# Optimization experiments

Measured on AMD Instinct MI355X. Metric: run time of the kernel, lower is better.

Reference implementation:

```python
import jax, jax.numpy as jnp
import numpy as np

C = 51  # num_relation


def setup_inputs() -> dict:
    key = jax.random.key(0)
    N_o, N_u, D = 16384, 16384, 1024
    k = jax.random.split(key, 6)
    feat = jax.random.normal(k[0], (N_o + N_u, D), jnp.float32)
    # first N_o rows are labeled (label != 0), remaining N_u rows unlabeled (label == 0)
    label = jnp.concatenate([
        jax.random.randint(k[1], (N_o,), 1, C),
        jnp.zeros((N_u,), jnp.int32),
    ]).astype(jnp.int32)
    W_o = jax.random.normal(k[2], (C, D), jnp.float32) * 0.03
    b_o = jnp.zeros((C,), jnp.float32)
    W = jax.random.normal(k[3], (C, D), jnp.float32) * 0.03
    b = jnp.zeros((C,), jnp.float32)
    cls = jnp.arange(C)
    group_mid_mask = (cls >= 16) & (cls < 36)   # groups[1]
    group_tail_mask = cls >= 36                 # groups[2]
    # runtime torch.randint partner sampling, hoisted to input construction
    idx_m = jax.random.randint(k[4], (2, N_u), 0, N_o)  # 2 mid copies
    idx_t = jax.random.randint(k[5], (3, N_u), 0, N_o)  # 3 tail copies
    return dict(feat=feat, label=label, W_o=W_o, b_o=b_o, W=W, b=b,
                group_mid_mask=group_mid_mask, group_tail_mask=group_tail_mask,
                idx_m=idx_m, idx_t=idx_t)


def reference(feat, label, W_o, b_o, W, b, group_mid_mask, group_tail_mask, idx_m, idx_t):
    n_u = idx_m.shape[1]
    n_o = feat.shape[0] - n_u
    feat_o, feat_u = feat[:n_o], feat[n_o:]
    label_o = label[:n_o]

    # fc_o under no_grad, then softmax / top-1 rank + score
    logits = jax.lax.stop_gradient(feat_u @ W_o.T + b_o)      # [N_u, C]
    p = jax.nn.softmax(logits, axis=1)
    pred = jnp.argmax(p, axis=1)                               # ranks[:,0]
    score = jnp.max(p, axis=1)                                 # score[:,0]

    # group membership + confidence thresholds (heads are unused in the original)
    mid_m = group_mid_mask[pred] & (score > 0.5)
    tail_m = group_tail_mask[pred] & (score > 0.3)

    oh_u = jax.nn.one_hot(pred, C, dtype=feat.dtype)
    oh_o = jax.nn.one_hot(label_o, C, dtype=feat.dtype)

    im = idx_m.reshape(-1)   # [2*N_u]
    it = idx_t.reshape(-1)   # [3*N_u]

    fm = 0.7 * feat_o[im] + 0.3 * jnp.tile(feat_u, (2, 1))
    lm = 0.7 * oh_o[im] + 0.3 * jnp.tile(oh_u, (2, 1))
    ft = 0.7 * feat_o[it] + 0.3 * jnp.tile(feat_u, (3, 1))
    lt = 0.7 * oh_o[it] + 0.3 * jnp.tile(oh_u, (3, 1))

    feat_cat = jnp.concatenate([fm, ft], axis=0)               # [5*N_u, D]
    label_cat = jnp.concatenate([lm, lt], axis=0)              # [5*N_u, C]
    w = jnp.concatenate([jnp.tile(mid_m, 2), jnp.tile(tail_m, 3)]).astype(feat.dtype)

    # soft-label cross entropy on fc(feat_cat); masked mean over selected rows
    logp = jax.nn.log_softmax(feat_cat @ W.T + b, axis=1)
    ce = -(logp * label_cat).sum(axis=1)
    cnt = w.sum()
    return (ce * w).sum() / jnp.maximum(cnt, 1.0)
```

## Files before the change

### kernel.cpp

```cpp
#include <hip/hip_runtime.h>
#include <math.h>

#define DD 1024
#define NU 16384
#define NO 16384

typedef short short8 __attribute__((ext_vector_type(8)));
typedef float f32x4 __attribute__((ext_vector_type(4)));

__device__ __forceinline__ unsigned short f2b(float x) {
    unsigned int u = __float_as_uint(x);
    u += 0x7FFFu + ((u >> 16) & 1u);
    return (unsigned short)(u >> 16);
}

__device__ __forceinline__ short8 cvt8(float4 a, float4 b) {
    short8 r;
    r[0] = (short)f2b(a.x); r[1] = (short)f2b(a.y);
    r[2] = (short)f2b(a.z); r[3] = (short)f2b(a.w);
    r[4] = (short)f2b(b.x); r[5] = (short)f2b(b.y);
    r[6] = (short)f2b(b.z); r[7] = (short)f2b(b.w);
    return r;
}

__global__ __launch_bounds__(256) void fused(const float* __restrict__ feat,
                                             const float* __restrict__ W_o,
                                             const float* __restrict__ b_o,
                                             const float* __restrict__ W,
                                             const float* __restrict__ bb,
                                             const int* __restrict__ label,
                                             const int* __restrict__ idxm,
                                             const int* __restrict__ idxt,
                                             double* __restrict__ pnum,
                                             int* __restrict__ pcnt) {
    __shared__ __attribute__((aligned(16))) unsigned short Bs[32][64][32];
    __shared__ int2 slist[192];
    __shared__ int scount;
    __shared__ float swsum[4];
    __shared__ int swcnt[4];

    const int tid = threadIdx.x;
    const int lane = tid & 63;
    const int w = tid >> 6;
    const int m = lane & 15;
    const int quad = lane >> 4;

    if (tid == 0) scount = 0;

#pragma unroll 8
    for (int i = tid; i < 51 * 256; i += 256) {
        const int row = i >> 8;
        const int c = i & 255;
        const int k0 = c * 4;
        const int kt = k0 >> 5;
        const int kl = k0 & 31;
        const int c4 = kl >> 3;
        const int half = (kl >> 2) & 1;
        const float4 v = *(const float4*)(W_o + (size_t)row * DD + k0);
        ushort4 o;
        o.x = f2b(v.x); o.y = f2b(v.y); o.z = f2b(v.z); o.w = f2b(v.w);
        char* dst = (char*)&Bs[kt][row][0] + ((c4 ^ (row & 3)) * 16 + half * 8);
        *(ushort4*)dst = o;
    }
#pragma unroll 4
    for (int i = tid; i < 13 * 256; i += 256) {
        const int row = 51 + (i >> 8);
        const int j = i & 255;
        char* dst = (char*)&Bs[j >> 3][row][0] + (j & 7) * 8;
        *(ushort4*)dst = make_ushort4(0, 0, 0, 0);
    }
    __syncthreads();

    const int urow = blockIdx.x * 64 + w * 16 + m;
    const char* abase = (const char*)(feat + (size_t)(NO + urow) * DD) + quad * 32;
    const int bswz = (quad ^ (m & 3)) * 16;

    f32x4 acc[4];
#pragma unroll
    for (int nf = 0; nf < 4; ++nf) acc[nf] = (f32x4){0.f, 0.f, 0.f, 0.f};

    float4 pa0[8], pa1[8];
#pragma unroll
    for (int t = 0; t < 8; ++t) {
        pa0[t] = *(const float4*)(abase + (size_t)t * 128);
        pa1[t] = *(const float4*)(abase + (size_t)t * 128 + 16);
    }
#pragma unroll
    for (int kt = 0; kt < 32; ++kt) {
        const int slot = kt & 7;
        const float4 f0 = pa0[slot];
        const float4 f1 = pa1[slot];
        if (kt < 24) {
            pa0[slot] = *(const float4*)(abase + (size_t)(kt + 8) * 128);
            pa1[slot] = *(const float4*)(abase + (size_t)(kt + 8) * 128 + 16);
        }
        const short8 af = cvt8(f0, f1);
#pragma unroll
        for (int nf = 0; nf < 4; ++nf) {
            const short8 bf =
                *(const short8*)((const char*)&Bs[kt][m + nf * 16][0] + bswz);
            acc[nf] = __builtin_amdgcn_mfma_f32_16x16x32_bf16(af, bf, acc[nf], 0, 0, 0);
        }
    }

    const int rloc = blockIdx.x * 64 + w * 16 + quad * 4;
    float boc[4];
#pragma unroll
    for (int c = 0; c < 4; ++c) {
        const int col = c * 16 + m;
        boc[c] = (col < 51) ? b_o[col] : 0.f;
    }
#pragma unroll
    for (int r = 0; r < 4; ++r) {
        float z[4];
        float mx = acc[0][r] + boc[0];
        int mi = m;
        z[0] = mx;
#pragma unroll
        for (int c = 1; c < 4; ++c) {
            const int col = c * 16 + m;
            z[c] = (col < 51) ? acc[c][r] + boc[c] : -INFINITY;
            if (z[c] > mx) { mx = z[c]; mi = col; }
        }
#pragma unroll
        for (int off = 1; off < 16; off <<= 1) {
            const float om = __shfl_xor(mx, off);
            const int oi = __shfl_xor(mi, off);
            if (om > mx || (om == mx && oi < mi)) { mx = om; mi = oi; }
        }
        float e = 0.f;
#pragma unroll
        for (int c = 0; c < 4; ++c)
            if (c * 16 + m < 51) e += expf(z[c] - mx);
#pragma unroll
        for (int off = 1; off < 16; off <<= 1) e += __shfl_xor(e, off);
        const float score = 1.f / e;
        const int mid = (mi >= 16 && mi < 36 && score > 0.5f) ? 1 : 0;
        const int tail = (mi >= 36 && score > 0.3f) ? 1 : 0;
        const int nref = mid ? 2 : (tail ? 3 : 0);
        if (m < nref) {
            const int u = rloc + r;
            const int oo = mid ? idxm[(size_t)m * NU + u]
                               : idxt[(size_t)m * NU + u];
            const int p = atomicAdd(&scount, 1);
            slist[p] = make_int2(oo, u | (mi << 16));
        }
    }
    __syncthreads();

    const int n = scount;
    const float bbv = (lane < 51) ? bb[lane] : 0.f;
    float fsum = 0.f;
    int ccnt = 0;
    for (int t = w; t < n; t += 4) {
        const int2 e = slist[t];
        const int ob = e.x;
        const int ub = e.y & 0xFFFF;
        const int pu = e.y >> 16;
        const f32x4* fo4 = (const f32x4*)(feat + (size_t)ob * DD);
        const f32x4* fu4 = (const f32x4*)(feat + (size_t)(NO + ub) * DD);
        f32x4 g[4];
#pragma unroll
        for (int q = 0; q < 4; ++q)
            g[q] = 0.7f * fo4[q * 64 + lane] + 0.3f * fu4[q * 64 + lane];
        float zmy = 0.f;
        for (int c = 0; c < 51; ++c) {
            const f32x4* wr = (const f32x4*)(W + (size_t)c * DD);
            f32x4 p = wr[lane] * g[0];
            p += wr[64 + lane] * g[1];
            p += wr[128 + lane] * g[2];
            p += wr[192 + lane] * g[3];
            float d = (p[0] + p[1]) + (p[2] + p[3]);
#pragma unroll
            for (int off = 1; off < 64; off <<= 1) d += __shfl_xor(d, off);
            if (lane == c) zmy = d;
        }
        const float z = (lane < 51) ? zmy + bbv : -INFINITY;
        float mx = z;
#pragma unroll
        for (int off = 1; off < 64; off <<= 1) mx = fmaxf(mx, __shfl_xor(mx, off));
        float e2 = (lane < 51) ? expf(z - mx) : 0.f;
#pragma unroll
        for (int off = 1; off < 64; off <<= 1) e2 += __shfl_xor(e2, off);
        const float lse = mx + logf(e2);
        const int lo = label[ob];
        const float zlo = __shfl(z, lo);
        const float zpu = __shfl(z, pu);
        fsum += lse - 0.7f * zlo - 0.3f * zpu;
        ++ccnt;
    }
    if (lane == 0) { swsum[w] = fsum; swcnt[w] = ccnt; }
    __syncthreads();
    if (tid == 0) {
        pnum[blockIdx.x] = (double)swsum[0] + (double)swsum[1] +
                           (double)swsum[2] + (double)swsum[3];
        pcnt[blockIdx.x] = swcnt[0] + swcnt[1] + swcnt[2] + swcnt[3];
    }
}

__global__ __launch_bounds__(256) void finalize(const double* __restrict__ pnum,
                                                const int* __restrict__ pcnt,
                                                float* __restrict__ out) {
    __shared__ double sd[4];
    __shared__ int sc[4];
    const int w = threadIdx.x >> 6;
    const int lane = threadIdx.x & 63;
    double s = pnum[threadIdx.x];
    int c = pcnt[threadIdx.x];
#pragma unroll
    for (int off = 1; off < 64; off <<= 1) {
        s += __shfl_xor(s, off);
        c += __shfl_xor(c, off);
    }
    if (lane == 0) { sd[w] = s; sc[w] = c; }
    __syncthreads();
    if (threadIdx.x == 0) {
        const double n = sd[0] + sd[1] + sd[2] + sd[3];
        const int cc = sc[0] + sc[1] + sc[2] + sc[3];
        out[0] = (float)(n / (cc > 1 ? (double)cc : 1.0));
    }
}

extern "C" void kernel_launch(void* const* d_in, const int* in_sizes, int n_in,
                              void* d_out, int out_size, void* d_ws, size_t ws_size,
                              hipStream_t stream) {
    const float* feat = (const float*)d_in[0];
    const int* label = (const int*)d_in[1];
    const float* W_o = (const float*)d_in[2];
    const float* b_o = (const float*)d_in[3];
    const float* W = (const float*)d_in[4];
    const float* b = (const float*)d_in[5];
    const int* idxm = (const int*)d_in[8];
    const int* idxt = (const int*)d_in[9];

    char* ws = (char*)d_ws;
    double* pnum = (double*)ws;
    int* pcnt = (int*)(ws + 2048);

    fused<<<256, 256, 0, stream>>>(feat, W_o, b_o, W, b, label, idxm, idxt,
                                   pnum, pcnt);
    finalize<<<1, 256, 0, stream>>>(pnum, pcnt, (float*)d_out);
}
```

Before: 222.8 us.

## Split the K dimension across four wave groups and widen blocks to 1024 threads

The fused kernel now launches 1024 threads per block instead of 256. Each of four wave groups handles a quarter of the 1024-wide K range of the first GEMM, and the partial accumulators are summed through shared memory before the argmax and softmax step. The mixup cross-entropy phase now spreads its selected rows over 16 waves instead of 4. Each thread's feature loads are issued before the barrier that follows the W_o staging, so they overlap with it. The aim is more waves per CU to hide memory latency, at the cost of a larger LDS footprint, an extra reduction pass and fewer registers per thread.

```diff
diff --git a/kernel.cpp b/kernel.cpp
--- a/kernel.cpp
+++ b/kernel.cpp
@@ -23,32 +23,34 @@
     return r;
 }
 
-__global__ __launch_bounds__(256) void fused(const float* __restrict__ feat,
-                                             const float* __restrict__ W_o,
-                                             const float* __restrict__ b_o,
-                                             const float* __restrict__ W,
-                                             const float* __restrict__ bb,
-                                             const int* __restrict__ label,
-                                             const int* __restrict__ idxm,
-                                             const int* __restrict__ idxt,
-                                             double* __restrict__ pnum,
-                                             int* __restrict__ pcnt) {
-    __shared__ __attribute__((aligned(16))) unsigned short Bs[32][64][32];
+__global__ __launch_bounds__(1024) void fused(const float* __restrict__ feat,
+                                              const float* __restrict__ W_o,
+                                              const float* __restrict__ b_o,
+                                              const float* __restrict__ W,
+                                              const float* __restrict__ bb,
+                                              const int* __restrict__ label,
+                                              const int* __restrict__ idxm,
+                                              const int* __restrict__ idxt,
+                                              double* __restrict__ pnum,
+                                              int* __restrict__ pcnt) {
+    __shared__ __attribute__((aligned(16))) char pool[131072];
     __shared__ int2 slist[192];
     __shared__ int scount;
-    __shared__ float swsum[4];
-    __shared__ int swcnt[4];
+    __shared__ float swsum[16];
+    __shared__ int swcnt[16];
 
     const int tid = threadIdx.x;
     const int lane = tid & 63;
     const int w = tid >> 6;
+    const int wg = w & 3;
+    const int kc = w >> 2;
     const int m = lane & 15;
     const int quad = lane >> 4;
 
     if (tid == 0) scount = 0;
 
-#pragma unroll 8
-    for (int i = tid; i < 51 * 256; i += 256) {
+#pragma unroll 4
+    for (int i = tid; i < 51 * 256; i += 1024) {
         const int row = i >> 8;
         const int c = i & 255;
         const int k0 = c * 4;
@@ -59,91 +61,100 @@
         const float4 v = *(const float4*)(W_o + (size_t)row * DD + k0);
         ushort4 o;
         o.x = f2b(v.x); o.y = f2b(v.y); o.z = f2b(v.z); o.w = f2b(v.w);
-        char* dst = (char*)&Bs[kt][row][0] + ((c4 ^ (row & 3)) * 16 + half * 8);
+        char* dst = pool + kt * 4096 + row * 64 + ((c4 ^ (row & 3)) * 16 + half * 8);
         *(ushort4*)dst = o;
     }
-#pragma unroll 4
-    for (int i = tid; i < 13 * 256; i += 256) {
-        const int row = 51 + (i >> 8);
-        const int j = i & 255;
-        char* dst = (char*)&Bs[j >> 3][row][0] + (j & 7) * 8;
-        *(ushort4*)dst = make_ushort4(0, 0, 0, 0);
-    }
-    __syncthreads();
-
-    const int urow = blockIdx.x * 64 + w * 16 + m;
-    const char* abase = (const char*)(feat + (size_t)(NO + urow) * DD) + quad * 32;
+
+    const int urow = blockIdx.x * 64 + wg * 16 + m;
+    const char* abase = (const char*)feat + (size_t)(NO + urow) * 4096
+                        + kc * 1024 + quad * 32;
+    float4 pa0[8], pa1[8];
+#pragma unroll
+    for (int t = 0; t < 8; ++t) {
+        pa0[t] = *(const float4*)(abase + t * 128);
+        pa1[t] = *(const float4*)(abase + t * 128 + 16);
+    }
+    __syncthreads();
+
     const int bswz = (quad ^ (m & 3)) * 16;
-
     f32x4 acc[4];
 #pragma unroll
     for (int nf = 0; nf < 4; ++nf) acc[nf] = (f32x4){0.f, 0.f, 0.f, 0.f};
-
-    float4 pa0[8], pa1[8];
-#pragma unroll
-    for (int t = 0; t < 8; ++t) {
-        pa0[t] = *(const float4*)(abase + (size_t)t * 128);
-        pa1[t] = *(const float4*)(abase + (size_t)t * 128 + 16);
-    }
-#pragma unroll
-    for (int kt = 0; kt < 32; ++kt) {
-        const int slot = kt & 7;
-        const float4 f0 = pa0[slot];
-        const float4 f1 = pa1[slot];
-        if (kt < 24) {
-            pa0[slot] = *(const float4*)(abase + (size_t)(kt + 8) * 128);
-            pa1[slot] = *(const float4*)(abase + (size_t)(kt + 8) * 128 + 16);
-        }
-        const short8 af = cvt8(f0, f1);
+#pragma unroll
+    for (int k = 0; k < 8; ++k) {
+        const short8 af = cvt8(pa0[k], pa1[k]);
+        const int kt = kc * 8 + k;
 #pragma unroll
         for (int nf = 0; nf < 4; ++nf) {
             const short8 bf =
-                *(const short8*)((const char*)&Bs[kt][m + nf * 16][0] + bswz);
+                *(const short8*)(pool + kt * 4096 + (m + nf * 16) * 64 + bswz);
             acc[nf] = __builtin_amdgcn_mfma_f32_16x16x32_bf16(af, bf, acc[nf], 0, 0, 0);
         }
     }
-
-    const int rloc = blockIdx.x * 64 + w * 16 + quad * 4;
-    float boc[4];
-#pragma unroll
-    for (int c = 0; c < 4; ++c) {
-        const int col = c * 16 + m;
-        boc[c] = (col < 51) ? b_o[col] : 0.f;
-    }
-#pragma unroll
-    for (int r = 0; r < 4; ++r) {
-        float z[4];
-        float mx = acc[0][r] + boc[0];
-        int mi = m;
-        z[0] = mx;
-#pragma unroll
-        for (int c = 1; c < 4; ++c) {
+    __syncthreads();
+
+    float* Rbuf = (float*)pool;
+#pragma unroll
+    for (int nf = 0; nf < 4; ++nf)
+#pragma unroll
+        for (int r = 0; r < 4; ++r)
+            Rbuf[(((kc * 4 + wg) * 16) + nf * 4 + r) * 64 + lane] = acc[nf][r];
+    __syncthreads();
+
+    if (kc == 0) {
+        float zz[4][4];
+#pragma unroll
+        for (int nf = 0; nf < 4; ++nf)
+#pragma unroll
+            for (int r = 0; r < 4; ++r) {
+                const int j = nf * 4 + r;
+                zz[nf][r] = Rbuf[((0 * 4 + wg) * 16 + j) * 64 + lane]
+                          + Rbuf[((1 * 4 + wg) * 16 + j) * 64 + lane]
+                          + Rbuf[((2 * 4 + wg) * 16 + j) * 64 + lane]
+                          + Rbuf[((3 * 4 + wg) * 16 + j) * 64 + lane];
+            }
+        const int rloc = blockIdx.x * 64 + wg * 16 + quad * 4;
+        float boc[4];
+#pragma unroll
+        for (int c = 0; c < 4; ++c) {
             const int col = c * 16 + m;
-            z[c] = (col < 51) ? acc[c][r] + boc[c] : -INFINITY;
-            if (z[c] > mx) { mx = z[c]; mi = col; }
-        }
-#pragma unroll
-        for (int off = 1; off < 16; off <<= 1) {
-            const float om = __shfl_xor(mx, off);
-            const int oi = __shfl_xor(mi, off);
-            if (om > mx || (om == mx && oi < mi)) { mx = om; mi = oi; }
-        }
-        float e = 0.f;
-#pragma unroll
-        for (int c = 0; c < 4; ++c)
-            if (c * 16 + m < 51) e += expf(z[c] - mx);
-#pragma unroll
-        for (int off = 1; off < 16; off <<= 1) e += __shfl_xor(e, off);
-        const float score = 1.f / e;
-        const int mid = (mi >= 16 && mi < 36 && score > 0.5f) ? 1 : 0;
-        const int tail = (mi >= 36 && score > 0.3f) ? 1 : 0;
-        const int nref = mid ? 2 : (tail ? 3 : 0);
-        if (m < nref) {
-            const int u = rloc + r;
-            const int oo = mid ? idxm[(size_t)m * NU + u]
-                               : idxt[(size_t)m * NU + u];
-            const int p = atomicAdd(&scount, 1);
-            slist[p] = make_int2(oo, u | (mi << 16));
+            boc[c] = (col < 51) ? b_o[col] : 0.f;
+        }
+#pragma unroll
+        for (int r = 0; r < 4; ++r) {
+            float z[4];
+            float mx = zz[0][r] + boc[0];
+            int mi = m;
+            z[0] = mx;
+#pragma unroll
+            for (int c = 1; c < 4; ++c) {
+                const int col = c * 16 + m;
+                z[c] = (col < 51) ? zz[c][r] + boc[c] : -INFINITY;
+                if (z[c] > mx) { mx = z[c]; mi = col; }
+            }
+#pragma unroll
+            for (int off = 1; off < 16; off <<= 1) {
+                const float om = __shfl_xor(mx, off);
+                const int oi = __shfl_xor(mi, off);
+                if (om > mx || (om == mx && oi < mi)) { mx = om; mi = oi; }
+            }
+            float e = 0.f;
+#pragma unroll
+            for (int c = 0; c < 4; ++c)
+                if (c * 16 + m < 51) e += expf(z[c] - mx);
+#pragma unroll
+            for (int off = 1; off < 16; off <<= 1) e += __shfl_xor(e, off);
+            const float score = 1.f / e;
+            const int mid = (mi >= 16 && mi < 36 && score > 0.5f) ? 1 : 0;
+            const int tail = (mi >= 36 && score > 0.3f) ? 1 : 0;
+            const int nref = mid ? 2 : (tail ? 3 : 0);
+            if (m < nref) {
+                const int u = rloc + r;
+                const int oo = mid ? idxm[(size_t)m * NU + u]
+                                   : idxt[(size_t)m * NU + u];
+                const int p = atomicAdd(&scount, 1);
+                slist[p] = make_int2(oo, u | (mi << 16));
+            }
         }
     }
     __syncthreads();
@@ -152,7 +163,7 @@
     const float bbv = (lane < 51) ? bb[lane] : 0.f;
     float fsum = 0.f;
     int ccnt = 0;
-    for (int t = w; t < n; t += 4) {
+    for (int t = w; t < n; t += 16) {
         const int2 e = slist[t];
         const int ob = e.x;
         const int ub = e.y & 0xFFFF;
@@ -192,9 +203,12 @@
     if (lane == 0) { swsum[w] = fsum; swcnt[w] = ccnt; }
     __syncthreads();
     if (tid == 0) {
-        pnum[blockIdx.x] = (double)swsum[0] + (double)swsum[1] +
-                           (double)swsum[2] + (double)swsum[3];
-        pcnt[blockIdx.x] = swcnt[0] + swcnt[1] + swcnt[2] + swcnt[3];
+        double bn = 0.0;
+        int bcnt = 0;
+#pragma unroll
+        for (int i = 0; i < 16; ++i) { bn += (double)swsum[i]; bcnt += swcnt[i]; }
+        pnum[blockIdx.x] = bn;
+        pcnt[blockIdx.x] = bcnt;
     }
 }
 
@@ -237,7 +251,7 @@
     double* pnum = (double*)ws;
     int* pcnt = (int*)(ws + 2048);
 
-    fused<<<256, 256, 0, stream>>>(feat, W_o, b_o, W, b, label, idxm, idxt,
-                                   pnum, pcnt);
+    fused<<<256, 1024, 0, stream>>>(feat, W_o, b_o, W, b, label, idxm, idxt,
+                                    pnum, pcnt);
     finalize<<<1, 256, 0, stream>>>(pnum, pcnt, (float*)d_out);
 }
```

Measured after the change: 220.3 us. No clear change (-1.1%).
